# Performance work log

Measured on AMD Instinct MI355X. Metric: run time of the kernel, lower is better.

The kernel has to match this reference:

```python
import jax, jax.numpy as jnp
import numpy as np
from functools import partial

B, S, D, L, O, V = 32, 1024, 256, 4, 64, 5  # batch, seq, d_model, n_layers, output_dim, vocab
EPS = 1e-5
RC_MAP = jnp.array([3, 2, 1, 0, 4], dtype=jnp.int32)  # A<->T, C<->G, N->N


def layernorm(x, g, b):
    m = jnp.mean(x, axis=-1, keepdims=True)
    v = jnp.mean((x - m) ** 2, axis=-1, keepdims=True)
    return (x - m) * jax.lax.rsqrt(v + EPS) * g + b


def gru(x, w_ih, w_hh, b_ih, b_hh):
    """torch nn.GRU (single layer, batch_first) equivalent.
    x: (B,S,D); w_ih: (3H,D); w_hh: (3H,H); gates ordered r,z,n."""
    H = w_hh.shape[1]
    # precompute input contributions for all timesteps: (S,B,3H)
    xi = (jnp.einsum('bsd,gd->bsg', x, w_ih) + b_ih).transpose(1, 0, 2)

    def step(h, xt):
        gh = h @ w_hh.T + b_hh                      # (B,3H)
        xr, xz, xn = jnp.split(xt, 3, axis=-1)
        hr, hz, hn = jnp.split(gh, 3, axis=-1)
        r = jax.nn.sigmoid(xr + hr)
        z = jax.nn.sigmoid(xz + hz)
        n = jnp.tanh(xn + r * hn)
        h2 = (1.0 - z) * n + z * h
        return h2, h2

    h0 = jnp.zeros((x.shape[0], H), dtype=x.dtype)
    _, out = jax.lax.scan(step, h0, xi)
    return out.transpose(1, 0, 2)                   # (B,S,H)


def setup_inputs() -> dict:
    key = jax.random.key(0)
    ks = jax.random.split(key, 32)
    n = lambda k, shp, s=0.02: (jax.random.normal(k, shp, dtype=jnp.float32) * s)
    inp = {
        'tokens': jax.random.randint(ks[0], (B, S), 0, V),
        'emb':    n(ks[1], (V, D), 1.0),
        'pos':    n(ks[2], (1, S, D)),
        # per-layer stacked params (leading dim L)
        'ln_g':   jnp.ones((L, D), jnp.float32),
        'ln_b':   jnp.zeros((L, D), jnp.float32),
        'wih_f':  n(ks[3], (L, 3 * D, D)),
        'whh_f':  n(ks[4], (L, 3 * D, D)),
        'bih_f':  n(ks[5], (L, 3 * D)),
        'bhh_f':  n(ks[6], (L, 3 * D)),
        'wih_r':  n(ks[7], (L, 3 * D, D)),
        'whh_r':  n(ks[8], (L, 3 * D, D)),
        'bih_r':  n(ks[9], (L, 3 * D)),
        'bhh_r':  n(ks[10], (L, 3 * D)),
        'wg':     n(ks[11], (L, D, 2 * D)),
        'bg':     n(ks[12], (L, D)),
        'wo':     n(ks[13], (L, D, D)),
        'bo':     n(ks[14], (L, D)),
        'fn_g':   jnp.ones((D,), jnp.float32),
        'fn_b':   jnp.zeros((D,), jnp.float32),
        'pw':     n(ks[15], (O, D)),
        'pb':     n(ks[16], (O,)),
        'pln_g':  jnp.ones((O,), jnp.float32),
        'pln_b':  jnp.zeros((O,), jnp.float32),
    }
    return inp


def reference(tokens, emb, pos, ln_g, ln_b,
              wih_f, whh_f, bih_f, bhh_f,
              wih_r, whh_r, bih_r, bhh_r,
              wg, bg, wo, bo, fn_g, fn_b, pw, pb, pln_g, pln_b):
    def encode(tok):
        h = emb[tok] + pos[:, :tok.shape[1], :]      # (B,S,D)
        for i in range(L):
            hn = layernorm(h, ln_g[i], ln_b[i])
            f = gru(hn, wih_f[i], whh_f[i], bih_f[i], bhh_f[i])
            r = jnp.flip(gru(jnp.flip(hn, 1), wih_r[i], whh_r[i], bih_r[i], bhh_r[i]), 1)
            g = jax.nn.sigmoid(jnp.concatenate([f, r], -1) @ wg[i].T + bg[i])
            c = g * f + (1.0 - g) * r
            h = c @ wo[i].T + bo[i] + h              # residual
        return layernorm(h, fn_g, fn_b)

    h = encode(tokens)
    rc_tokens = jnp.flip(RC_MAP[tokens], -1)         # reverse-complement
    h_rc = encode(rc_tokens)
    pooled = (h.mean(1) + h_rc.mean(1)) * 0.5        # (B,D)
    p = layernorm(pooled @ pw.T + pb, pln_g, pln_b)
    return jax.nn.gelu(p, approximate=False)         # (B,O)
```

## Files before the change

### kernel.cpp

```cpp
#include <hip/hip_runtime.h>
#include <stdint.h>

#define DEV __device__ __forceinline__

typedef unsigned short u16;
typedef __attribute__((ext_vector_type(8))) __bf16 bf16x8;
typedef __attribute__((ext_vector_type(4))) float f32x4;

DEV float bf2f(u16 u) {
    unsigned v = ((unsigned)u) << 16;
    float f;
    __builtin_memcpy(&f, &v, 4);
    return f;
}
DEV u16 f2bf(float x) {
    unsigned u;
    __builtin_memcpy(&u, &x, 4);
    return (u16)((u + 0x7FFFu + ((u >> 16) & 1u)) >> 16);
}
DEV float sigf(float x) {
    float e = __builtin_amdgcn_exp2f(-1.442695040888963f * x);
    return __builtin_amdgcn_rcpf(1.0f + e);
}
DEV float tanhf_(float x) {
    float e = __builtin_amdgcn_exp2f(2.885390081777927f * x);
    return (e - 1.0f) * __builtin_amdgcn_rcpf(e + 1.0f);
}
DEV f32x4 mfma16(bf16x8 a, bf16x8 b, f32x4 c) {
    return __builtin_amdgcn_mfma_f32_16x16x32_bf16(a, b, c, 0, 0, 0);
}

static constexpr size_t XROW = 1536;
static constexpr size_t XE = 32768 * XROW;

__global__ void convert_w(const float* __restrict__ src, u16* __restrict__ dst,
                          int n_per, int stride_l, int total) {
    int idx = blockIdx.x * 256 + threadIdx.x;
    if (idx >= total) return;
    int l = idx / n_per;
    int r = idx - l * n_per;
    dst[(size_t)l * stride_l + r] = f2bf(src[idx]);
}

__global__ void convert_wih(const float* __restrict__ src, const float* __restrict__ lng,
                            u16* __restrict__ dst, int dir_ofs) {
    int idx = blockIdx.x * 256 + threadIdx.x;
    int l = idx / 196608;
    int r = idx - l * 196608;
    int k = idx & 255;
    dst[(size_t)l * 393216 + dir_ofs + r] = f2bf(src[idx] * lng[l * 256 + k]);
}

__global__ void head_vecs_kernel(const float* __restrict__ wihf, const float* __restrict__ wihr,
                                 const float* __restrict__ bihf, const float* __restrict__ bihr,
                                 const float* __restrict__ bhhf, const float* __restrict__ bhhr,
                                 const float* __restrict__ lng, const float* __restrict__ lnb,
                                 float* __restrict__ env, float* __restrict__ cvec) {
    int w = threadIdx.x >> 6, lane = threadIdx.x & 63;
    int row = blockIdx.x * 4 + w;
    int l = row / 1536;
    int n1536 = row - l * 1536;
    int dir = n1536 >= 768;
    int n = n1536 - dir * 768;
    const float* W = (dir ? wihr : wihf) + ((size_t)l * 768 + n) * 256 + lane * 4;
    float4 wv = *(const float4*)W;
    float4 gv = *(const float4*)(lng + l * 256 + lane * 4);
    float4 bv = *(const float4*)(lnb + l * 256 + lane * 4);
    float es = wv.x * gv.x + wv.y * gv.y + wv.z * gv.z + wv.w * gv.w;
    float cs = wv.x * bv.x + wv.y * bv.y + wv.z * bv.z + wv.w * bv.w;
#pragma unroll
    for (int off = 1; off < 64; off <<= 1) {
        es += __shfl_xor(es, off);
        cs += __shfl_xor(cs, off);
    }
    if (lane == 0) {
        env[row] = es;
        float c = cs + (dir ? bihr : bihf)[l * 768 + n];
        if (n < 512) c += (dir ? bhhr : bhhf)[l * 768 + n];
        cvec[row] = c;
    }
}

__global__ void embed_kernel(const int* __restrict__ tok, const float* __restrict__ emb,
                             const float* __restrict__ pos, u16* __restrict__ h) {
    int row = blockIdx.x;
    int k = threadIdx.x;
    int e = row >> 15;
    int rem = row & 32767;
    int b = rem >> 10;
    int s = rem & 1023;
    int t0 = (e == 0) ? tok[b * 1024 + s] : tok[b * 1024 + (1023 - s)];
    if (e == 1) t0 = (t0 < 4) ? (3 - t0) : 4;
    h[(size_t)row * 256 + k] = f2bf(emb[t0 * 256 + k] + pos[s * 256 + k]);
}

__global__ void ln_stats_kernel(const u16* __restrict__ h, float2* __restrict__ stats) {
    int w = threadIdx.x >> 6, lane = threadIdx.x & 63;
    int row = blockIdx.x * 4 + w;
    int e = row >> 15;
    int rem = row & 32767;
    int b = rem >> 10;
    int s = rem & 1023;
    ushort4 v = *(const ushort4*)(h + (size_t)row * 256 + lane * 4);
    float x0 = bf2f(v.x), x1 = bf2f(v.y), x2 = bf2f(v.z), x3 = bf2f(v.w);
    float sum = x0 + x1 + x2 + x3;
    float sq = x0 * x0 + x1 * x1 + x2 * x2 + x3 * x3;
#pragma unroll
    for (int off = 1; off < 64; off <<= 1) {
        sum += __shfl_xor(sum, off);
        sq += __shfl_xor(sq, off);
    }
    if (lane == 0) {
        float mean = sum * (1.0f / 256.0f);
        float var = sq * (1.0f / 256.0f) - mean * mean;
        stats[e * 32768 + s * 32 + b] = make_float2(mean, rsqrtf(var + 1e-5f));
    }
}

template <int OP>
__global__ __launch_bounds__(256, 2) void gemm_bt(
    const u16* __restrict__ hin, const u16* __restrict__ Bw,
    const float* __restrict__ bias0, const float* __restrict__ bias1,
    u16* xibuf, const float2* __restrict__ stats, u16* hres) {
    constexpr int KK = (OP == 1) ? 512 : 256;
    constexpr int NKB = KK / 64;
    __shared__ __align__(16) u16 As[2][128 * 64];
    __shared__ __align__(16) u16 Bs[2][128 * 64];
    const int tid = threadIdx.x;
    const int lane = tid & 63, w = tid >> 6;
    const int l15 = lane & 15, q = lane >> 4;
    const int l8 = lane & 7, r8 = lane >> 3;
    const int e = blockIdx.z;
    const int m0 = blockIdx.x * 128, n0 = blockIdx.y * 128;
    const int wm = w & 1, wn = w >> 1;

    uint4 ra[4], rb[4];
    auto loadS = [&](int kb) {
#pragma unroll
        for (int i = 0; i < 4; ++i) {
            int row = w * 32 + i * 8 + r8;
            int c = l8 ^ (row & 7);
            int mrow = m0 + row;
            const u16* ap;
            if constexpr (OP == 0) {
                int bb = mrow & 31, ss = mrow >> 5;
                ap = hin + ((size_t)e * 32768 + bb * 1024 + ss) * 256 + kb * 64;
            } else if constexpr (OP == 1) {
                int colbase = (kb >= 4) ? 768 : 0;
                ap = xibuf + (size_t)e * XE + (size_t)mrow * XROW + colbase + (kb & 3) * 64;
            } else {
                ap = xibuf + (size_t)e * XE + (size_t)mrow * XROW + 256 + kb * 64;
            }
            ra[i] = *(const uint4*)(ap + c * 8);
            rb[i] = *(const uint4*)(Bw + (size_t)(n0 + row) * KK + kb * 64 + c * 8);
        }
    };
    auto writeS = [&](int buf) {
#pragma unroll
        for (int i = 0; i < 4; ++i) {
            int row = w * 32 + i * 8 + r8;
            *(uint4*)&As[buf][row * 64 + l8 * 8] = ra[i];
            *(uint4*)&Bs[buf][row * 64 + l8 * 8] = rb[i];
        }
    };

    f32x4 acc[4][4];
#pragma unroll
    for (int i = 0; i < 4; ++i)
#pragma unroll
        for (int j = 0; j < 4; ++j) acc[i][j] = (f32x4){0.f, 0.f, 0.f, 0.f};

    loadS(0);
    writeS(0);
    for (int kb = 0; kb < NKB; ++kb) {
        if (kb + 1 < NKB) loadS(kb + 1);
        __syncthreads();
        const int buf = kb & 1;
#pragma unroll
        for (int kt = 0; kt < 2; ++kt) {
            bf16x8 af[4], bfr[4];
#pragma unroll
            for (int i = 0; i < 4; ++i) {
                int rowa = wm * 64 + i * 16 + l15;
                int rowb = wn * 64 + i * 16 + l15;
                int c = kt * 4 + q;
                af[i] = *(const bf16x8*)&As[buf][rowa * 64 + (c ^ (rowa & 7)) * 8];
                bfr[i] = *(const bf16x8*)&Bs[buf][rowb * 64 + (c ^ (rowb & 7)) * 8];
            }
#pragma unroll
            for (int i = 0; i < 4; ++i)
#pragma unroll
                for (int j = 0; j < 4; ++j) acc[i][j] = mfma16(af[i], bfr[j], acc[i][j]);
        }
        if (kb + 1 < NKB) writeS((kb + 1) & 1);
    }

#pragma unroll
    for (int i = 0; i < 4; ++i) {
        const int mb = m0 + wm * 64 + i * 16 + q * 4;
        float2 st[4];
        if constexpr (OP == 0) {
#pragma unroll
            for (int r = 0; r < 4; ++r) st[r] = stats[e * 32768 + mb + r];
        }
#pragma unroll
        for (int jt = 0; jt < 4; ++jt) {
            const int nn = n0 + wn * 64 + jt * 16 + l15;
            f32x4 a = acc[i][jt];
            if constexpr (OP == 0) {
                const float en = bias0[nn], cn = bias1[nn];
#pragma unroll
                for (int r = 0; r < 4; ++r) {
                    float val = a[r] * st[r].y - st[r].x * st[r].y * en + cn;
                    xibuf[(size_t)e * XE + (size_t)(mb + r) * XROW + nn] = f2bf(val);
                }
            } else if constexpr (OP == 1) {
                const float bs = bias0[nn];
#pragma unroll
                for (int r = 0; r < 4; ++r) {
                    u16* xr_ = xibuf + (size_t)e * XE + (size_t)(mb + r) * XROW;
                    float gg = sigf(a[r] + bs);
                    float fv = bf2f(xr_[nn]), rv = bf2f(xr_[768 + nn]);
                    xr_[256 + nn] = f2bf(gg * fv + (1.0f - gg) * rv);
                }
            } else {
                const float bs = bias0[nn];
#pragma unroll
                for (int r = 0; r < 4; ++r) {
                    const int mm = mb + r;
                    size_t idx = ((size_t)e * 32768 + (size_t)(mm & 31) * 1024 + (mm >> 5)) * 256 + nn;
                    hres[idx] = f2bf(bf2f(hres[idx]) + a[r] + bs);
                }
            }
        }
    }
}

__global__ __launch_bounds__(512, 2) void scan_kernel(
    u16* xi, const u16* __restrict__ whh,
    const float* __restrict__ bhhf, const float* __restrict__ bhhr) {
    __shared__ __align__(16) u16 h_lds[16 * 264];
    const int tid = threadIdx.x;
    const int w = tid >> 6, lane = tid & 63;
    const int l15 = lane & 15, q = lane >> 4;
    const int bid = blockIdx.x;
    const int bh = bid & 1, d = (bid >> 1) & 1, e = bid >> 2;
    const int jb = w * 32;

    const u16* W = whh + (size_t)d * 196608;
    bf16x8 wf[3][2][8];
#pragma unroll
    for (int g = 0; g < 3; ++g)
#pragma unroll
        for (int jc = 0; jc < 2; ++jc)
#pragma unroll
            for (int kt = 0; kt < 8; ++kt)
                wf[g][jc][kt] = *(const bf16x8*)(
                    W + (size_t)(g * 256 + jb + jc * 16 + l15) * 256 + kt * 32 + q * 8);

    const float* bnp = (d ? bhhr : bhhf) + 512;
    f32x4 bn[2];
#pragma unroll
    for (int jc = 0; jc < 2; ++jc)
#pragma unroll
        for (int r = 0; r < 4; ++r) bn[jc][r] = bnp[jb + jc * 16 + q * 4 + r];

    const int s0 = d ? 1023 : 0;
    const ptrdiff_t step = (d ? -32 : 32) * (ptrdiff_t)XROW;
    u16* p = xi + (size_t)e * XE + (size_t)(s0 * 32 + bh * 16 + l15) * XROW + d * 768 + jb + q * 4;

    const int lrow = l15 * 264;
    const int jcol = jb + q * 4;

    ushort4 xvv[3][2];
#pragma unroll
    for (int g = 0; g < 3; ++g)
#pragma unroll
        for (int jc = 0; jc < 2; ++jc)
            xvv[g][jc] = *(const ushort4*)(p + g * 256 + jc * 16);

    for (int t = 0; t < 1024; ++t) {
        f32x4 a0[2], a1[2], a2[2];
#pragma unroll
        for (int jc = 0; jc < 2; ++jc) {
            a0[jc] = (f32x4){0.f, 0.f, 0.f, 0.f};
            a1[jc] = (f32x4){0.f, 0.f, 0.f, 0.f};
            a2[jc] = bn[jc];
        }
        if (t > 0) {
#pragma unroll
            for (int kt = 0; kt < 8; ++kt) {
                bf16x8 hb = *(const bf16x8*)&h_lds[lrow + kt * 32 + q * 8];
#pragma unroll
                for (int jc = 0; jc < 2; ++jc) {
                    a0[jc] = mfma16(wf[0][jc][kt], hb, a0[jc]);
                    a1[jc] = mfma16(wf[1][jc][kt], hb, a1[jc]);
                    a2[jc] = mfma16(wf[2][jc][kt], hb, a2[jc]);
                }
            }
        }
        ushort4 hs[2];
#pragma unroll
        for (int jc = 0; jc < 2; ++jc) {
            ushort4 hp4 = (t > 0) ? *(const ushort4*)&h_lds[lrow + jcol + jc * 16]
                                  : (ushort4){0, 0, 0, 0};
            u16 hr[4];
#pragma unroll
            for (int r = 0; r < 4; ++r) {
                float xr = bf2f(((const u16*)&xvv[0][jc])[r]);
                float xz = bf2f(((const u16*)&xvv[1][jc])[r]);
                float xn = bf2f(((const u16*)&xvv[2][jc])[r]);
                float rg = sigf(xr + a0[jc][r]);
                float zg = sigf(xz + a1[jc][r]);
                float ng = tanhf_(__builtin_fmaf(rg, a2[jc][r], xn));
                float hp = (t > 0) ? bf2f(((const u16*)&hp4)[r]) : 0.f;
                float h2 = __builtin_fmaf(zg, hp - ng, ng);
                hr[r] = f2bf(h2);
            }
            hs[jc] = (ushort4){hr[0], hr[1], hr[2], hr[3]};
        }
        *(ushort4*)(p + 0) = hs[0];
        *(ushort4*)(p + 16) = hs[1];
        __syncthreads();
        *(ushort4*)&h_lds[lrow + jcol] = hs[0];
        *(ushort4*)&h_lds[lrow + jcol + 16] = hs[1];
        __syncthreads();
        if (t + 1 < 1024) {
            p += step;
#pragma unroll
            for (int g = 0; g < 3; ++g)
#pragma unroll
                for (int jc = 0; jc < 2; ++jc)
                    xvv[g][jc] = *(const ushort4*)(p + g * 256 + jc * 16);
        }
    }
}

__global__ __launch_bounds__(256) void pool_head_kernel(
    const u16* __restrict__ h, const float* __restrict__ fng, const float* __restrict__ fnb,
    const float* __restrict__ pw, const float* __restrict__ pb,
    const float* __restrict__ plng, const float* __restrict__ plnb, float* __restrict__ out) {
    __shared__ float pacc[4][256];
    __shared__ float pooled[256];
    const int b = blockIdx.x;
    const int tid = threadIdx.x;
    const int w = tid >> 6, lane = tid & 63;
    float a0 = 0.f, a1 = 0.f, a2 = 0.f, a3 = 0.f;
    for (int rr = w; rr < 2048; rr += 4) {
        int e = rr >> 10, s = rr & 1023;
        const u16* src = h + ((size_t)e * 32768 + (size_t)b * 1024 + s) * 256 + lane * 4;
        ushort4 v = *(const ushort4*)src;
        float x0 = bf2f(v.x), x1 = bf2f(v.y), x2 = bf2f(v.z), x3 = bf2f(v.w);
        float sum = x0 + x1 + x2 + x3;
        float sq = x0 * x0 + x1 * x1 + x2 * x2 + x3 * x3;
#pragma unroll
        for (int off = 1; off < 64; off <<= 1) {
            sum += __shfl_xor(sum, off);
            sq += __shfl_xor(sq, off);
        }
        float mean = sum * (1.0f / 256.0f);
        float var = sq * (1.0f / 256.0f) - mean * mean;
        float rs = rsqrtf(var + 1e-5f);
        a0 += (x0 - mean) * rs;
        a1 += (x1 - mean) * rs;
        a2 += (x2 - mean) * rs;
        a3 += (x3 - mean) * rs;
    }
    pacc[w][lane * 4 + 0] = a0;
    pacc[w][lane * 4 + 1] = a1;
    pacc[w][lane * 4 + 2] = a2;
    pacc[w][lane * 4 + 3] = a3;
    __syncthreads();
    {
        int k = tid;
        float t = pacc[0][k] + pacc[1][k] + pacc[2][k] + pacc[3][k];
        pooled[k] = (t * fng[k] + 2048.0f * fnb[k]) * (0.5f / 1024.0f);
    }
    __syncthreads();
    if (tid < 64) {
        float p = pb[tid];
        const float* wrow = pw + tid * 256;
        for (int k = 0; k < 256; ++k) p += pooled[k] * wrow[k];
        float sum = p;
#pragma unroll
        for (int off = 1; off < 64; off <<= 1) sum += __shfl_xor(sum, off);
        float mean = sum * (1.0f / 64.0f);
        float dv = p - mean;
        float sq = dv * dv;
#pragma unroll
        for (int off = 1; off < 64; off <<= 1) sq += __shfl_xor(sq, off);
        float var = sq * (1.0f / 64.0f);
        float y = dv * rsqrtf(var + 1e-5f) * plng[tid] + plnb[tid];
        out[b * 64 + tid] = y * 0.5f * (1.0f + erff(y * 0.70710678118654752f));
    }
}

extern "C" void kernel_launch(void* const* d_in, const int* in_sizes, int n_in,
                              void* d_out, int out_size, void* d_ws, size_t ws_size,
                              hipStream_t stream) {
    (void)in_sizes; (void)n_in; (void)out_size; (void)ws_size;
    const int* tokens = (const int*)d_in[0];
    const float* emb = (const float*)d_in[1];
    const float* pos = (const float*)d_in[2];
    const float* ln_g = (const float*)d_in[3];
    const float* ln_b = (const float*)d_in[4];
    const float* wih_f = (const float*)d_in[5];
    const float* whh_f = (const float*)d_in[6];
    const float* bih_f = (const float*)d_in[7];
    const float* bhh_f = (const float*)d_in[8];
    const float* wih_r = (const float*)d_in[9];
    const float* whh_r = (const float*)d_in[10];
    const float* bih_r = (const float*)d_in[11];
    const float* bhh_r = (const float*)d_in[12];
    const float* wg = (const float*)d_in[13];
    const float* bg = (const float*)d_in[14];
    const float* wo = (const float*)d_in[15];
    const float* bo = (const float*)d_in[16];
    const float* fn_g = (const float*)d_in[17];
    const float* fn_b = (const float*)d_in[18];
    const float* pw = (const float*)d_in[19];
    const float* pb = (const float*)d_in[20];
    const float* pln_g = (const float*)d_in[21];
    const float* pln_b = (const float*)d_in[22];
    float* out = (float*)d_out;
    char* ws = (char*)d_ws;

    u16* h = (u16*)(ws + 0);
    u16* xi = (u16*)(ws + 33554432);
    u16* wih_cat = (u16*)(ws + 234881024);
    u16* whh_bf = (u16*)(ws + 238026752);
    u16* wg_bf = (u16*)(ws + 241172480);
    u16* wo_bf = (u16*)(ws + 242221056);
    float* env = (float*)(ws + 242745344);
    float* cvec = (float*)(ws + 242769920);
    float2* stats = (float2*)(ws + 242794496);

    convert_wih<<<3072, 256, 0, stream>>>(wih_f, ln_g, wih_cat, 0);
    convert_wih<<<3072, 256, 0, stream>>>(wih_r, ln_g, wih_cat, 196608);
    convert_w<<<3072, 256, 0, stream>>>(whh_f, whh_bf, 196608, 393216, 786432);
    convert_w<<<3072, 256, 0, stream>>>(whh_r, whh_bf + 196608, 196608, 393216, 786432);
    convert_w<<<2048, 256, 0, stream>>>(wg, wg_bf, 131072, 131072, 524288);
    convert_w<<<1024, 256, 0, stream>>>(wo, wo_bf, 65536, 65536, 262144);
    head_vecs_kernel<<<1536, 256, 0, stream>>>(wih_f, wih_r, bih_f, bih_r, bhh_f, bhh_r,
                                               ln_g, ln_b, env, cvec);
    embed_kernel<<<65536, 256, 0, stream>>>(tokens, emb, pos, h);

    for (int i = 0; i < 4; ++i) {
        ln_stats_kernel<<<16384, 256, 0, stream>>>(h, stats);
        gemm_bt<0><<<dim3(256, 12, 2), 256, 0, stream>>>(
            h, wih_cat + (size_t)i * 393216, env + i * 1536, cvec + i * 1536,
            xi, stats, nullptr);
        scan_kernel<<<8, 512, 0, stream>>>(
            xi, whh_bf + (size_t)i * 393216, bhh_f + i * 768, bhh_r + i * 768);
        gemm_bt<1><<<dim3(256, 2, 2), 256, 0, stream>>>(
            nullptr, wg_bf + (size_t)i * 131072, bg + i * 256, nullptr,
            xi, nullptr, nullptr);
        gemm_bt<2><<<dim3(256, 2, 2), 256, 0, stream>>>(
            nullptr, wo_bf + (size_t)i * 65536, bo + i * 256, nullptr,
            xi, nullptr, h);
    }
    pool_head_kernel<<<32, 256, 0, stream>>>(h, fn_g, fn_b, pw, pb, pln_g, pln_b, out);
}
```

Measured before the change: 10.44 ms.

## Double-buffer GRU hidden state, fold exp2 scales into weights, keep h in registers

```diff
diff --git a/kernel.cpp b/kernel.cpp
--- a/kernel.cpp
+++ b/kernel.cpp
@@ -22,16 +22,14 @@
     float e = __builtin_amdgcn_exp2f(-1.442695040888963f * x);
     return __builtin_amdgcn_rcpf(1.0f + e);
 }
-DEV float tanhf_(float x) {
-    float e = __builtin_amdgcn_exp2f(2.885390081777927f * x);
-    return (e - 1.0f) * __builtin_amdgcn_rcpf(e + 1.0f);
-}
 DEV f32x4 mfma16(bf16x8 a, bf16x8 b, f32x4 c) {
     return __builtin_amdgcn_mfma_f32_16x16x32_bf16(a, b, c, 0, 0, 0);
 }
 
 static constexpr size_t XROW = 1536;
 static constexpr size_t XE = 32768 * XROW;
+static constexpr float NL2E = -1.442695040888963f;
+static constexpr float P2L2E = 2.885390081777927f;
 
 __global__ void convert_w(const float* __restrict__ src, u16* __restrict__ dst,
                           int n_per, int stride_l, int total) {
@@ -42,13 +40,22 @@
     dst[(size_t)l * stride_l + r] = f2bf(src[idx]);
 }
 
+__global__ void convert_whh(const float* __restrict__ src, u16* __restrict__ dst, int dir_ofs) {
+    int idx = blockIdx.x * 256 + threadIdx.x;
+    int l = idx / 196608;
+    int r = idx - l * 196608;
+    float S = ((r >> 16) < 2) ? NL2E : P2L2E;
+    dst[(size_t)l * 393216 + dir_ofs + r] = f2bf(src[idx] * S);
+}
+
 __global__ void convert_wih(const float* __restrict__ src, const float* __restrict__ lng,
                             u16* __restrict__ dst, int dir_ofs) {
     int idx = blockIdx.x * 256 + threadIdx.x;
     int l = idx / 196608;
     int r = idx - l * 196608;
     int k = idx & 255;
-    dst[(size_t)l * 393216 + dir_ofs + r] = f2bf(src[idx] * lng[l * 256 + k]);
+    float S = ((r >> 16) < 2) ? NL2E : P2L2E;
+    dst[(size_t)l * 393216 + dir_ofs + r] = f2bf(src[idx] * lng[l * 256 + k] * S);
 }
 
 __global__ void head_vecs_kernel(const float* __restrict__ wihf, const float* __restrict__ wihr,
@@ -74,10 +81,11 @@
         cs += __shfl_xor(cs, off);
     }
     if (lane == 0) {
-        env[row] = es;
+        float S = (n < 512) ? NL2E : P2L2E;
         float c = cs + (dir ? bihr : bihf)[l * 768 + n];
         if (n < 512) c += (dir ? bhhr : bhhf)[l * 768 + n];
-        cvec[row] = c;
+        env[row] = es * S;
+        cvec[row] = c * S;
     }
 }
 
@@ -236,10 +244,10 @@
     }
 }
 
-__global__ __launch_bounds__(512, 2) void scan_kernel(
+__global__ __launch_bounds__(512, 1) void scan_kernel(
     u16* xi, const u16* __restrict__ whh,
     const float* __restrict__ bhhf, const float* __restrict__ bhhr) {
-    __shared__ __align__(16) u16 h_lds[16 * 264];
+    __shared__ __align__(16) u16 h_lds[2][16 * 264];
     const int tid = threadIdx.x;
     const int w = tid >> 6, lane = tid & 63;
     const int l15 = lane & 15, q = lane >> 4;
@@ -263,7 +271,7 @@
 #pragma unroll
     for (int jc = 0; jc < 2; ++jc)
 #pragma unroll
-        for (int r = 0; r < 4; ++r) bn[jc][r] = bnp[jb + jc * 16 + q * 4 + r];
+        for (int r = 0; r < 4; ++r) bn[jc][r] = P2L2E * bnp[jb + jc * 16 + q * 4 + r];
 
     const int s0 = d ? 1023 : 0;
     const ptrdiff_t step = (d ? -32 : 32) * (ptrdiff_t)XROW;
@@ -279,7 +287,11 @@
         for (int jc = 0; jc < 2; ++jc)
             xvv[g][jc] = *(const ushort4*)(p + g * 256 + jc * 16);
 
+    float hprev[2][4] = {{0.f, 0.f, 0.f, 0.f}, {0.f, 0.f, 0.f, 0.f}};
+
     for (int t = 0; t < 1024; ++t) {
+        const u16* rbuf = h_lds[(t & 1) ^ 1];
+        u16* wbuf = h_lds[t & 1];
         f32x4 a0[2], a1[2], a2[2];
 #pragma unroll
         for (int jc = 0; jc < 2; ++jc) {
@@ -290,7 +302,7 @@
         if (t > 0) {
 #pragma unroll
             for (int kt = 0; kt < 8; ++kt) {
-                bf16x8 hb = *(const bf16x8*)&h_lds[lrow + kt * 32 + q * 8];
+                bf16x8 hb = *(const bf16x8*)&rbuf[lrow + kt * 32 + q * 8];
 #pragma unroll
                 for (int jc = 0; jc < 2; ++jc) {
                     a0[jc] = mfma16(wf[0][jc][kt], hb, a0[jc]);
@@ -302,29 +314,27 @@
         ushort4 hs[2];
 #pragma unroll
         for (int jc = 0; jc < 2; ++jc) {
-            ushort4 hp4 = (t > 0) ? *(const ushort4*)&h_lds[lrow + jcol + jc * 16]
-                                  : (ushort4){0, 0, 0, 0};
             u16 hr[4];
 #pragma unroll
             for (int r = 0; r < 4; ++r) {
                 float xr = bf2f(((const u16*)&xvv[0][jc])[r]);
                 float xz = bf2f(((const u16*)&xvv[1][jc])[r]);
                 float xn = bf2f(((const u16*)&xvv[2][jc])[r]);
-                float rg = sigf(xr + a0[jc][r]);
-                float zg = sigf(xz + a1[jc][r]);
-                float ng = tanhf_(__builtin_fmaf(rg, a2[jc][r], xn));
-                float hp = (t > 0) ? bf2f(((const u16*)&hp4)[r]) : 0.f;
-                float h2 = __builtin_fmaf(zg, hp - ng, ng);
+                float rg = __builtin_amdgcn_rcpf(1.0f + __builtin_amdgcn_exp2f(xr + a0[jc][r]));
+                float zg = __builtin_amdgcn_rcpf(1.0f + __builtin_amdgcn_exp2f(xz + a1[jc][r]));
+                float E = __builtin_amdgcn_exp2f(__builtin_fmaf(rg, a2[jc][r], xn));
+                float ng = (E - 1.0f) * __builtin_amdgcn_rcpf(E + 1.0f);
+                float h2 = __builtin_fmaf(zg, hprev[jc][r] - ng, ng);
+                hprev[jc][r] = h2;
                 hr[r] = f2bf(h2);
             }
             hs[jc] = (ushort4){hr[0], hr[1], hr[2], hr[3]};
         }
+        *(ushort4*)&wbuf[lrow + jcol] = hs[0];
+        *(ushort4*)&wbuf[lrow + jcol + 16] = hs[1];
+        __syncthreads();
         *(ushort4*)(p + 0) = hs[0];
         *(ushort4*)(p + 16) = hs[1];
-        __syncthreads();
-        *(ushort4*)&h_lds[lrow + jcol] = hs[0];
-        *(ushort4*)&h_lds[lrow + jcol + 16] = hs[1];
-        __syncthreads();
         if (t + 1 < 1024) {
             p += step;
 #pragma unroll
@@ -437,8 +447,8 @@
 
     convert_wih<<<3072, 256, 0, stream>>>(wih_f, ln_g, wih_cat, 0);
     convert_wih<<<3072, 256, 0, stream>>>(wih_r, ln_g, wih_cat, 196608);
-    convert_w<<<3072, 256, 0, stream>>>(whh_f, whh_bf, 196608, 393216, 786432);
-    convert_w<<<3072, 256, 0, stream>>>(whh_r, whh_bf + 196608, 196608, 393216, 786432);
+    convert_whh<<<3072, 256, 0, stream>>>(whh_f, whh_bf, 0);
+    convert_whh<<<3072, 256, 0, stream>>>(whh_r, whh_bf, 196608);
     convert_w<<<2048, 256, 0, stream>>>(wg, wg_bf, 131072, 131072, 524288);
     convert_w<<<1024, 256, 0, stream>>>(wo, wo_bf, 65536, 65536, 262144);
     head_vecs_kernel<<<1536, 256, 0, stream>>>(wih_f, wih_r, bih_f, bih_r, bhh_f, bhh_r,
```

After: 14.05 ms. +34.5%, slower.
